# Optimization experiments

Measured on AMD Instinct MI355X. Metric: run time of the kernel, lower is better.

The kernel has to match this reference:

```python
import jax, jax.numpy as jnp
import numpy as np
import math

NUM_HEADS = 16
MAX_REL_POS = 128


def setup_inputs() -> dict:
    key = jax.random.key(0)
    ks = jax.random.split(key, 6)
    B, S, H = 4, 1024, 1024
    hd = H // NUM_HEADS
    sc = 1.0 / math.sqrt(H)
    return {
        "x": jax.random.normal(ks[0], (B, S, H), jnp.float32),
        "Wq": jax.random.normal(ks[1], (H, H), jnp.float32) * sc,
        "bq": jnp.zeros((H,), jnp.float32),
        "Wk": jax.random.normal(ks[2], (H, H), jnp.float32) * sc,
        "bk": jnp.zeros((H,), jnp.float32),
        "Wv": jax.random.normal(ks[3], (H, H), jnp.float32) * sc,
        "bv": jnp.zeros((H,), jnp.float32),
        "Wo": jax.random.normal(ks[4], (H, H), jnp.float32) * sc,
        "bo": jnp.zeros((H,), jnp.float32),
        "rel_emb": jax.random.normal(ks[5], (2 * MAX_REL_POS + 1, hd), jnp.float32) * 0.02,
    }


def reference(x, Wq, bq, Wk, bk, Wv, bv, Wo, bo, rel_emb):
    B, S, H = x.shape
    nh = NUM_HEADS
    hd = H // nh
    inv_sqrt_d = 1.0 / math.sqrt(hd)

    # torch Linear: y = x @ W.T + b; reshape to [B, nh, S, hd]
    def proj(W, b):
        return (x @ W.T + b).reshape(B, S, nh, hd).transpose(0, 2, 1, 3)

    Q = proj(Wq, bq)
    K = proj(Wk, bk)
    V = proj(Wv, bv)

    # relative position indices, clipped to [-max_rel_pos, max_rel_pos]
    pos = jnp.arange(S)
    rel_idx = jnp.clip(pos[None, :] - pos[:, None], -MAX_REL_POS, MAX_REL_POS) + MAX_REL_POS
    E = rel_emb[rel_idx]  # [S, S, hd]

    # content scores + learned relative-position bias, both scaled by 1/sqrt(hd)
    scores = (jnp.einsum('bnqd,bnkd->bnqk', Q, K)
              + jnp.einsum('bnqd,qkd->bnqk', Q, E)) * inv_sqrt_d
    attn = jax.nn.softmax(scores, axis=-1)

    out = jnp.einsum('bnqk,bnkd->bnqd', attn, V)  # [B, nh, S, hd]
    out = out.transpose(0, 2, 1, 3).reshape(B, S, H)
    return out @ Wo.T + bo
```

## Files before the change

### kernel.cpp

```cpp
#include <hip/hip_runtime.h>
#include <math.h>

#define S_LEN 1024
#define NREL  257
#define QRST  272

typedef _Float16 f16;
typedef __attribute__((ext_vector_type(8))) _Float16 f16x8;
typedef __attribute__((ext_vector_type(4))) float f32x4;

__device__ inline void load_lds_16(const void* g, void* l) {
    __builtin_amdgcn_global_load_lds(
        (const __attribute__((address_space(1))) void*)g,
        (__attribute__((address_space(3))) void*)l, 16, 0, 0);
}

__global__ __launch_bounds__(256)
void convert_f16(const float* __restrict__ src, f16* __restrict__ dst)
{
    const int t = blockIdx.x * 256 + threadIdx.x;
    const int row128 = t & 127;
    const int kc     = (t >> 7) & 3;
    const int ktile  = (t >> 9) & 31;
    const int mtile  = t >> 14;
    const float* s = src + ((size_t)(mtile * 128 + row128) * 1024) + ktile * 32 + kc * 8;
    float4 v0 = *reinterpret_cast<const float4*>(s);
    float4 v1 = *reinterpret_cast<const float4*>(s + 4);
    float v[8] = {v0.x, v0.y, v0.z, v0.w, v1.x, v1.y, v1.z, v1.w};
    union { f16 h[8]; int4 q; } H;
    #pragma unroll
    for (int i = 0; i < 8; ++i) H.h[i] = (f16)v[i];
    reinterpret_cast<int4*>(dst)[t] = H.q;
}

__global__ __launch_bounds__(256)
void convert_w(const float* __restrict__ Wq, const float* __restrict__ Wk,
               const float* __restrict__ Wv, const float* __restrict__ Wo,
               f16* __restrict__ wqkv, f16* __restrict__ wo)
{
    const int y = blockIdx.y;
    const float* src = (y == 0) ? Wq : (y == 1) ? Wk : (y == 2) ? Wv : Wo;
    f16* dst = (y < 3) ? (wqkv + (size_t)y * 1048576) : wo;
    const int t = blockIdx.x * 256 + threadIdx.x;
    const int row128 = t & 127;
    const int kc     = (t >> 7) & 3;
    const int ktile  = (t >> 9) & 31;
    const int mtile  = t >> 14;
    const float* s = src + ((size_t)(mtile * 128 + row128) * 1024) + ktile * 32 + kc * 8;
    float4 v0 = *reinterpret_cast<const float4*>(s);
    float4 v1 = *reinterpret_cast<const float4*>(s + 4);
    float v[8] = {v0.x, v0.y, v0.z, v0.w, v1.x, v1.y, v1.z, v1.w};
    union { f16 h[8]; int4 q; } H;
    #pragma unroll
    for (int i = 0; i < 8; ++i) H.h[i] = (f16)v[i];
    reinterpret_cast<int4*>(dst)[t] = H.q;
}

__global__ __launch_bounds__(256)
void rel_convert(const float* __restrict__ rel, f16* __restrict__ relc)
{
    const int t = blockIdx.x * 256 + threadIdx.x;
    const int ck = t / 272, row = t % 272;
    union { f16 h[8]; int4 q; } H;
    #pragma unroll
    for (int i = 0; i < 8; ++i) H.h[i] = (f16)0.f;
    if (ck < 8 && row < NREL) {
        const float* s = rel + (size_t)row * 64 + ck * 8;
        float4 v0 = *reinterpret_cast<const float4*>(s);
        float4 v1 = *reinterpret_cast<const float4*>(s + 4);
        float v[8] = {v0.x, v0.y, v0.z, v0.w, v1.x, v1.y, v1.z, v1.w};
        #pragma unroll
        for (int i = 0; i < 8; ++i) H.h[i] = (f16)v[i];
    }
    reinterpret_cast<int4*>(relc)[t] = H.q;
}

__global__ __launch_bounds__(256)
void gemm_qkv(const f16* __restrict__ Ah, const f16* __restrict__ Bh,
              const float* __restrict__ bq, const float* __restrict__ bk,
              const float* __restrict__ bv,
              f16* __restrict__ Qout, f16* __restrict__ Kt, f16* __restrict__ Vt)
{
    __shared__ __align__(16) f16 sm[2][2][4096];
    const int tid  = threadIdx.x;
    const int wave = tid >> 6, lane = tid & 63;
    const int wm = wave >> 1, wn = wave & 1;
    const int r16 = lane & 15, kq = lane >> 4;
    const int mtile = blockIdx.y;
    const int ntile = blockIdx.x;
    const int wb = (tid & ~63) << 3;

    f32x4 acc[4][4] = {};

    auto stage = [&](int buf, int kt) {
        const f16* gA = Ah + ((size_t)(mtile * 32 + kt) << 12);
        const f16* gB = Bh + ((size_t)(ntile * 32 + kt) << 12);
        load_lds_16(gA + ((size_t)tid << 3),         &sm[buf][0][wb]);
        load_lds_16(gA + ((size_t)(tid + 256) << 3), &sm[buf][0][wb + 2048]);
        load_lds_16(gB + ((size_t)tid << 3),         &sm[buf][1][wb]);
        load_lds_16(gB + ((size_t)(tid + 256) << 3), &sm[buf][1][wb + 2048]);
    };

    stage(0, 0);
    __syncthreads();

    for (int kt = 0; kt < 32; ++kt) {
        const int cur = kt & 1;
        if (kt + 1 < 32) stage(cur ^ 1, kt + 1);

        const f16x8* pA = reinterpret_cast<const f16x8*>(sm[cur][0]);
        const f16x8* pB = reinterpret_cast<const f16x8*>(sm[cur][1]);

        f16x8 af[4], bf[4];
        #pragma unroll
        for (int m = 0; m < 4; ++m) af[m] = pA[kq * 128 + wm * 64 + m * 16 + r16];
        #pragma unroll
        for (int n = 0; n < 4; ++n) bf[n] = pB[kq * 128 + wn * 64 + n * 16 + r16];
        #pragma unroll
        for (int m = 0; m < 4; ++m)
            #pragma unroll
            for (int n = 0; n < 4; ++n)
                acc[m][n] = __builtin_amdgcn_mfma_f32_16x16x32_f16(af[m], bf[n], acc[m][n], 0, 0, 0);
        __syncthreads();
    }

    const int nsel = ntile >> 3;
    const float scale = (nsel == 0) ? 0.125f : 1.0f;
    const float* bp = (nsel == 0) ? bq : ((nsel == 1) ? bk : bv);
    const int row0 = (mtile << 7) + wm * 64;
    const int col0 = ((ntile & 7) << 7) + wn * 64;

    #pragma unroll
    for (int n = 0; n < 4; ++n) {
        const int col = col0 + n * 16 + r16;
        const float bc = bp[col];
        #pragma unroll
        for (int m = 0; m < 4; ++m) {
            #pragma unroll
            for (int r = 0; r < 4; ++r) {
                const int row = row0 + m * 16 + kq * 4 + r;
                const float val = (acc[m][n][r] + bc) * scale;
                const int b = row >> 10, s = row & 1023;
                const int nh = col >> 6, d = col & 63;
                if (nsel == 0) {
                    Qout[((((size_t)(b * 16 + nh)) << 10 | (size_t)s) << 6) + d] = (f16)val;
                } else if (nsel == 1) {
                    const size_t cidx = (((size_t)(b * 16 + nh) << 13) + ((s >> 6) << 9)
                                        + ((d >> 3) << 6) + (s & 63)) * 8 + (d & 7);
                    Kt[cidx] = (f16)val;
                } else {
                    const int kk = s & 63;
                    const size_t cidx = (((size_t)(b * 16 + nh) << 13) + ((s >> 6) << 9)
                                        + ((kk >> 3) << 6) + d) * 8 + (kk & 7);
                    Vt[cidx] = (f16)val;
                }
            }
        }
    }
}

__global__ __launch_bounds__(256)
void gemm_out(const f16* __restrict__ Ah, const f16* __restrict__ Bh,
              const float* __restrict__ bias, float* __restrict__ out)
{
    __shared__ __align__(16) f16 sm[2][6144];
    const int tid  = threadIdx.x;
    const int wave = tid >> 6, lane = tid & 63;
    const int wm = wave >> 1, wn = wave & 1;
    const int r16 = lane & 15, kq = lane >> 4;
    const int mtile = blockIdx.y;
    const int ntile = blockIdx.x;
    const int wb = (tid & ~63) << 3;

    f32x4 acc[4][2] = {};

    auto stage = [&](int buf, int kt) {
        const f16* gA = Ah + ((size_t)(mtile * 32 + kt) << 12);
        const f16* gB = Bh + ((size_t)((ntile >> 1) * 32 + kt) << 12) + ((ntile & 1) << 9);
        load_lds_16(gA + ((size_t)tid << 3),         &sm[buf][wb]);
        load_lds_16(gA + ((size_t)(tid + 256) << 3), &sm[buf][wb + 2048]);
        load_lds_16(gB + (((size_t)(tid >> 6)) << 10) + ((size_t)(tid & 63) << 3),
                    &sm[buf][4096 + wb]);
    };

    stage(0, 0);
    __syncthreads();

    for (int kt = 0; kt < 32; ++kt) {
        const int cur = kt & 1;
        if (kt + 1 < 32) stage(cur ^ 1, kt + 1);

        const f16x8* pA = reinterpret_cast<const f16x8*>(&sm[cur][0]);
        const f16x8* pB = reinterpret_cast<const f16x8*>(&sm[cur][4096]);

        f16x8 af[4], bf[2];
        #pragma unroll
        for (int m = 0; m < 4; ++m) af[m] = pA[kq * 128 + wm * 64 + m * 16 + r16];
        #pragma unroll
        for (int n = 0; n < 2; ++n) bf[n] = pB[kq * 64 + wn * 32 + n * 16 + r16];
        #pragma unroll
        for (int m = 0; m < 4; ++m)
            #pragma unroll
            for (int n = 0; n < 2; ++n)
                acc[m][n] = __builtin_amdgcn_mfma_f32_16x16x32_f16(af[m], bf[n], acc[m][n], 0, 0, 0);
        __syncthreads();
    }

    const int row0 = (mtile << 7) + wm * 64;
    const int col0 = (ntile << 6) + wn * 32;
    #pragma unroll
    for (int n = 0; n < 2; ++n) {
        const int col = col0 + n * 16 + r16;
        const float bc = bias[col];
        #pragma unroll
        for (int m = 0; m < 4; ++m)
            #pragma unroll
            for (int r = 0; r < 4; ++r) {
                const int row = row0 + m * 16 + kq * 4 + r;
                out[(size_t)row * 1024 + col] = acc[m][n][r] + bc;
            }
    }
}

__global__ __launch_bounds__(256)
void qrel_gemm(const f16* __restrict__ Qf, const f16* __restrict__ relc,
               f16* __restrict__ QR)
{
    __shared__ __align__(16) char lds[36864];
    const int tid = threadIdx.x;
    const int w = tid >> 6, l = tid & 63;
    const int r16 = l & 15, kq = l >> 4;
    const int blk = blockIdx.x;
    const int wb = (tid & 192) << 4;

    #pragma unroll
    for (int i = 0; i < 9; ++i)
        load_lds_16((const char*)relc + i * 4096 + tid * 16, lds + i * 4096 + wb);

    const int qrow = (blk << 6) + w * 16 + r16;
    f16x8 ah[2];
    ah[0] = *reinterpret_cast<const f16x8*>(Qf + (size_t)qrow * 64 + kq * 8);
    ah[1] = *reinterpret_cast<const f16x8*>(Qf + (size_t)qrow * 64 + 32 + kq * 8);

    __syncthreads();

    f32x4 S[17] = {};
    const f16x8* cB = reinterpret_cast<const f16x8*>(lds);
    #pragma unroll
    for (int c = 0; c < 2; ++c) {
        #pragma unroll
        for (int n = 0; n < 17; ++n) {
            const f16x8 bf = cB[(c * 4 + kq) * 272 + n * 16 + r16];
            S[n] = __builtin_amdgcn_mfma_f32_16x16x32_f16(ah[c], bf, S[n], 0, 0, 0);
        }
    }

    const int qbase = (blk << 6) + w * 16 + kq * 4;
    #pragma unroll
    for (int n = 0; n < 17; ++n) {
        const int col = n * 16 + r16;
        #pragma unroll
        for (int r = 0; r < 4; ++r)
            QR[(size_t)(qbase + r) * QRST + col] = (f16)S[n][r];
    }
}

__global__ __launch_bounds__(256, 2)
void attn_kernel(const f16* __restrict__ Qf, const f16* __restrict__ Kt,
                 const f16* __restrict__ Vt, const f16* __restrict__ QR,
                 f16* __restrict__ AO)
{
    __shared__ __align__(16) char lds[16384 + 128 * 68 * 4];
    float* P = (float*)(lds + 16384);

    const int id  = blockIdx.x;
    const int xcd = id & 7;
    const int j   = id >> 3;
    const int qt  = j & 7;
    const int bh  = ((j >> 3) << 3) | xcd;
    const int q0  = qt << 7;

    const int tid = threadIdx.x;
    const int w = tid >> 6;
    const int l = tid & 63;
    const int r16 = l & 15, kq = l >> 4;

    f16x8 qf[2][2];
    #pragma unroll
    for (int m = 0; m < 2; ++m) {
        const size_t qoff = (((size_t)bh << 10) + q0 + w * 32 + m * 16 + r16) * 64;
        #pragma unroll
        for (int c = 0; c < 2; ++c)
            qf[m][c] = *reinterpret_cast<const f16x8*>(Qf + qoff + c * 32 + kq * 8);
    }

    float qr_lo[2][4], qr_hi[2][4];
    #pragma unroll
    for (int m = 0; m < 2; ++m)
        #pragma unroll
        for (int r = 0; r < 4; ++r) {
            const f16* p = QR + (size_t)((bh << 10) + q0 + w * 32 + m * 16 + kq * 4 + r) * QRST;
            qr_lo[m][r] = (float)p[0];
            qr_hi[m][r] = (float)p[256];
        }

    float m_run[2][4] = {{-1e30f, -1e30f, -1e30f, -1e30f}, {-1e30f, -1e30f, -1e30f, -1e30f}};
    float l_run[2][4] = {};
    f32x4 accO[2][4] = {};

    const int wb = (tid & 192) << 4;

    for (int kt = 0; kt < S_LEN; kt += 64) {
        __syncthreads();

        {
            const size_t tbase = ((size_t)(bh * 16) + (kt >> 6)) * 8192;
            const char* gK = (const char*)Kt + tbase;
            const char* gV = (const char*)Vt + tbase;
            #pragma unroll
            for (int i = 0; i < 2; ++i) {
                load_lds_16(gK + i * 4096 + tid * 16, lds + i * 4096 + wb);
                load_lds_16(gV + i * 4096 + tid * 16, lds + 8192 + i * 4096 + wb);
            }
        }

        float bias[2][4][4];
        if (kt - q0 >= 256) {
            #pragma unroll
            for (int m = 0; m < 2; ++m)
                #pragma unroll
                for (int n = 0; n < 4; ++n)
                    #pragma unroll
                    for (int r = 0; r < 4; ++r) bias[m][n][r] = qr_hi[m][r];
        } else if (q0 - kt >= 192) {
            #pragma unroll
            for (int m = 0; m < 2; ++m)
                #pragma unroll
                for (int n = 0; n < 4; ++n)
                    #pragma unroll
                    for (int r = 0; r < 4; ++r) bias[m][n][r] = qr_lo[m][r];
        } else {
            #pragma unroll
            for (int m = 0; m < 2; ++m) {
                const int qb = q0 + w * 32 + m * 16 + kq * 4;
                const int base_d = kt - qb + 128 + r16;
                #pragma unroll
                for (int r = 0; r < 4; ++r) {
                    const f16* qrp = QR + (size_t)((bh << 10) + qb + r) * QRST;
                    #pragma unroll
                    for (int n = 0; n < 4; ++n) {
                        int dlt = base_d + n * 16 - r;
                        dlt = dlt < 0 ? 0 : (dlt > 256 ? 256 : dlt);
                        bias[m][n][r] = (float)qrp[dlt];
                    }
                }
            }
        }

        __syncthreads();

        f32x4 S[2][4] = {};
        const f16x8* cK = reinterpret_cast<const f16x8*>(lds);
        #pragma unroll
        for (int c = 0; c < 2; ++c) {
            f16x8 kf[4];
            #pragma unroll
            for (int n = 0; n < 4; ++n)
                kf[n] = cK[(c * 4 + kq) * 64 + n * 16 + r16];
            #pragma unroll
            for (int m = 0; m < 2; ++m)
                #pragma unroll
                for (int n = 0; n < 4; ++n)
                    S[m][n] = __builtin_amdgcn_mfma_f32_16x16x32_f16(qf[m][c], kf[n], S[m][n], 0, 0, 0);
        }

        #pragma unroll
        for (int m = 0; m < 2; ++m) {
            float pv[4][4];
            float tmax[4] = {-1e30f, -1e30f, -1e30f, -1e30f};
            #pragma unroll
            for (int n = 0; n < 4; ++n)
                #pragma unroll
                for (int r = 0; r < 4; ++r) {
                    const float s = S[m][n][r] + bias[m][n][r];
                    pv[n][r] = s;
                    tmax[r] = fmaxf(tmax[r], s);
                }
            #pragma unroll
            for (int r = 0; r < 4; ++r) {
                tmax[r] = fmaxf(tmax[r], __shfl_xor(tmax[r], 1));
                tmax[r] = fmaxf(tmax[r], __shfl_xor(tmax[r], 2));
                tmax[r] = fmaxf(tmax[r], __shfl_xor(tmax[r], 4));
                tmax[r] = fmaxf(tmax[r], __shfl_xor(tmax[r], 8));
            }
            float corr[4], psum[4] = {0.f, 0.f, 0.f, 0.f};
            #pragma unroll
            for (int r = 0; r < 4; ++r) {
                const float m_new = fmaxf(m_run[m][r], tmax[r]);
                corr[r] = __expf(m_run[m][r] - m_new);
                m_run[m][r] = m_new;
            }
            #pragma unroll
            for (int n = 0; n < 4; ++n)
                #pragma unroll
                for (int r = 0; r < 4; ++r) {
                    pv[n][r] = __expf(pv[n][r] - m_run[m][r]);
                    psum[r] += pv[n][r];
                }
            #pragma unroll
            for (int r = 0; r < 4; ++r) {
                psum[r] += __shfl_xor(psum[r], 1);
                psum[r] += __shfl_xor(psum[r], 2);
                psum[r] += __shfl_xor(psum[r], 4);
                psum[r] += __shfl_xor(psum[r], 8);
                l_run[m][r] = l_run[m][r] * corr[r] + psum[r];
            }
            #pragma unroll
            for (int n = 0; n < 4; ++n)
                #pragma unroll
                for (int r = 0; r < 4; ++r) accO[m][n][r] *= corr[r];

            #pragma unroll
            for (int n = 0; n < 4; ++n)
                #pragma unroll
                for (int r = 0; r < 4; ++r)
                    P[(w * 32 + m * 16 + kq * 4 + r) * 68 + n * 16 + r16] = pv[n][r];
        }

        __syncthreads();

        const f16x8* cV = reinterpret_cast<const f16x8*>(lds + 8192);
        #pragma unroll
        for (int m = 0; m < 2; ++m) {
            const int prow = (w * 32 + m * 16 + r16) * 68;
            #pragma unroll
            for (int c = 0; c < 2; ++c) {
                float4 p0 = *reinterpret_cast<const float4*>(&P[prow + c * 32 + kq * 8]);
                float4 p1 = *reinterpret_cast<const float4*>(&P[prow + c * 32 + kq * 8 + 4]);
                f16x8 pa;
                pa[0] = (f16)p0.x; pa[1] = (f16)p0.y; pa[2] = (f16)p0.z; pa[3] = (f16)p0.w;
                pa[4] = (f16)p1.x; pa[5] = (f16)p1.y; pa[6] = (f16)p1.z; pa[7] = (f16)p1.w;
                #pragma unroll
                for (int n = 0; n < 4; ++n) {
                    const f16x8 vf = cV[(c * 4 + kq) * 64 + n * 16 + r16];
                    accO[m][n] = __builtin_amdgcn_mfma_f32_16x16x32_f16(pa, vf, accO[m][n], 0, 0, 0);
                }
            }
        }
    }

    #pragma unroll
    for (int m = 0; m < 2; ++m) {
        float inv[4];
        #pragma unroll
        for (int r = 0; r < 4; ++r) inv[r] = 1.f / l_run[m][r];
        const int qs_base = q0 + w * 32 + m * 16 + kq * 4;
        #pragma unroll
        for (int n = 0; n < 4; ++n)
            #pragma unroll
            for (int r = 0; r < 4; ++r) {
                const float v = accO[m][n][r] * inv[r];
                const int r_g  = ((bh >> 4) << 10) + qs_base + r;
                const int kcol = ((bh & 15) << 6) + n * 16 + r16;
                const size_t idx = ((((size_t)(r_g >> 7) * 32 + (kcol >> 5)) * 4
                                    + ((kcol >> 3) & 3)) * 128 + (r_g & 127)) * 8 + (kcol & 7);
                AO[idx] = (f16)v;
            }
    }
}

extern "C" void kernel_launch(void* const* d_in, const int* in_sizes, int n_in,
                              void* d_out, int out_size, void* d_ws, size_t ws_size,
                              hipStream_t stream)
{
    const float* x   = (const float*)d_in[0];
    const float* Wq  = (const float*)d_in[1];
    const float* bq  = (const float*)d_in[2];
    const float* Wk  = (const float*)d_in[3];
    const float* bk  = (const float*)d_in[4];
    const float* Wv  = (const float*)d_in[5];
    const float* bv  = (const float*)d_in[6];
    const float* Wo  = (const float*)d_in[7];
    const float* bo  = (const float*)d_in[8];
    const float* rel = (const float*)d_in[9];
    float* out = (float*)d_out;

    char* W = (char*)d_ws;
    f16* Qf   = (f16*)(W);
    f16* QR   = (f16*)(W + 8388608);
    f16* Kt   = (f16*)(W + 44040192);
    f16* Vt   = (f16*)(W + 52428800);
    f16* xt   = (f16*)(W + 60817408);
    f16* wqkv = (f16*)(W + 69206016);
    f16* wo   = (f16*)(W + 75497472);
    f16* AO   = (f16*)(W + 77594624);
    f16* relc = (f16*)(W + 85983232);

    convert_f16<<<2048, 256, 0, stream>>>(x, xt);
    convert_w<<<dim3(512, 4), 256, 0, stream>>>(Wq, Wk, Wv, Wo, wqkv, wo);
    rel_convert<<<9, 256, 0, stream>>>(rel, relc);

    gemm_qkv<<<dim3(24, 32), dim3(256), 0, stream>>>(
        xt, wqkv, bq, bk, bv, Qf, Kt, Vt);

    qrel_gemm<<<1024, 256, 0, stream>>>(Qf, relc, QR);

    attn_kernel<<<512, 256, 0, stream>>>(Qf, Kt, Vt, QR, AO);

    gemm_out<<<dim3(16, 32), dim3(256), 0, stream>>>(AO, wo, bo, out);
}
```

Baseline: 258.5 us.

## Double-buffer K/V tiles, prefetch bias, store P as f16, MFMA row sums

Restructures the attention loop so the next K/V tile is loaded into a second LDS buffer and its relative-position bias is gathered while the current tile is computed. This removes one block barrier per iteration and hides global load latency. The softmax probabilities are now written to LDS as f16 instead of f32, halving P traffic and dropping the per-read conversion. The row-sum shuffle reduction is replaced by an extra MFMA against a ones vector. The trade-off is roughly 51 KB of LDS per block instead of about 51 KB split differently, more live registers for the prefetched bias, and a row sum taken from f16-rounded probabilities.

After: 219.3 us. -15.2%, faster.

```diff
diff --git a/kernel.cpp b/kernel.cpp
--- a/kernel.cpp
+++ b/kernel.cpp
@@ -270,8 +270,8 @@
                  const f16* __restrict__ Vt, const f16* __restrict__ QR,
                  f16* __restrict__ AO)
 {
-    __shared__ __align__(16) char lds[16384 + 128 * 68 * 4];
-    float* P = (float*)(lds + 16384);
+    __shared__ __align__(16) char lds[32768 + 128 * 72 * 2];
+    f16* Pf = (f16*)(lds + 32768);
 
     const int id  = blockIdx.x;
     const int xcd = id & 7;
@@ -284,6 +284,7 @@
     const int w = tid >> 6;
     const int l = tid & 63;
     const int r16 = l & 15, kq = l >> 4;
+    const int wb = (tid & 192) << 4;
 
     f16x8 qf[2][2];
     #pragma unroll
@@ -305,45 +306,41 @@
         }
 
     float m_run[2][4] = {{-1e30f, -1e30f, -1e30f, -1e30f}, {-1e30f, -1e30f, -1e30f, -1e30f}};
-    float l_run[2][4] = {};
     f32x4 accO[2][4] = {};
-
-    const int wb = (tid & 192) << 4;
-
-    for (int kt = 0; kt < S_LEN; kt += 64) {
-        __syncthreads();
-
-        {
-            const size_t tbase = ((size_t)(bh * 16) + (kt >> 6)) * 8192;
-            const char* gK = (const char*)Kt + tbase;
-            const char* gV = (const char*)Vt + tbase;
-            #pragma unroll
-            for (int i = 0; i < 2; ++i) {
-                load_lds_16(gK + i * 4096 + tid * 16, lds + i * 4096 + wb);
-                load_lds_16(gV + i * 4096 + tid * 16, lds + 8192 + i * 4096 + wb);
-            }
-        }
-
-        float bias[2][4][4];
-        if (kt - q0 >= 256) {
+    f32x4 acc_l[2] = {};
+
+    auto stage = [&](int buf, int t) {
+        const size_t tbase = ((size_t)(bh * 16) + t) * 8192;
+        const char* gK = (const char*)Kt + tbase;
+        const char* gV = (const char*)Vt + tbase;
+        #pragma unroll
+        for (int i = 0; i < 2; ++i) {
+            load_lds_16(gK + i * 4096 + tid * 16, lds + buf * 16384 + i * 4096 + wb);
+            load_lds_16(gV + i * 4096 + tid * 16, lds + buf * 16384 + 8192 + i * 4096 + wb);
+        }
+    };
+
+    auto gather = [&](int t, float (&bb)[2][4][4]) {
+        const int ktv = t << 6;
+        if (ktv - q0 >= 256) {
             #pragma unroll
             for (int m = 0; m < 2; ++m)
                 #pragma unroll
                 for (int n = 0; n < 4; ++n)
                     #pragma unroll
-                    for (int r = 0; r < 4; ++r) bias[m][n][r] = qr_hi[m][r];
-        } else if (q0 - kt >= 192) {
+                    for (int r = 0; r < 4; ++r) bb[m][n][r] = qr_hi[m][r];
+        } else if (q0 - ktv >= 192) {
             #pragma unroll
             for (int m = 0; m < 2; ++m)
                 #pragma unroll
                 for (int n = 0; n < 4; ++n)
                     #pragma unroll
-                    for (int r = 0; r < 4; ++r) bias[m][n][r] = qr_lo[m][r];
+                    for (int r = 0; r < 4; ++r) bb[m][n][r] = qr_lo[m][r];
         } else {
             #pragma unroll
             for (int m = 0; m < 2; ++m) {
                 const int qb = q0 + w * 32 + m * 16 + kq * 4;
-                const int base_d = kt - qb + 128 + r16;
+                const int base_d = ktv - qb + 128 + r16;
                 #pragma unroll
                 for (int r = 0; r < 4; ++r) {
                     const f16* qrp = QR + (size_t)((bh << 10) + qb + r) * QRST;
@@ -351,16 +348,31 @@
                     for (int n = 0; n < 4; ++n) {
                         int dlt = base_d + n * 16 - r;
                         dlt = dlt < 0 ? 0 : (dlt > 256 ? 256 : dlt);
-                        bias[m][n][r] = (float)qrp[dlt];
+                        bb[m][n][r] = (float)qrp[dlt];
                     }
                 }
             }
         }
-
-        __syncthreads();
+    };
+
+    float biasc[2][4][4];
+    stage(0, 0);
+    gather(0, biasc);
+    __syncthreads();
+
+    const f16x8 ones = {(f16)1.f, (f16)1.f, (f16)1.f, (f16)1.f,
+                        (f16)1.f, (f16)1.f, (f16)1.f, (f16)1.f};
+
+    for (int t = 0; t < 16; ++t) {
+        const int cur = t & 1;
+        float nb[2][4][4];
+        if (t + 1 < 16) {
+            stage(cur ^ 1, t + 1);
+            gather(t + 1, nb);
+        }
 
         f32x4 S[2][4] = {};
-        const f16x8* cK = reinterpret_cast<const f16x8*>(lds);
+        const f16x8* cK = reinterpret_cast<const f16x8*>(lds + cur * 16384);
         #pragma unroll
         for (int c = 0; c < 2; ++c) {
             f16x8 kf[4];
@@ -382,7 +394,7 @@
             for (int n = 0; n < 4; ++n)
                 #pragma unroll
                 for (int r = 0; r < 4; ++r) {
-                    const float s = S[m][n][r] + bias[m][n][r];
+                    const float s = S[m][n][r] + biasc[m][n][r];
                     pv[n][r] = s;
                     tmax[r] = fmaxf(tmax[r], s);
                 }
@@ -393,7 +405,7 @@
                 tmax[r] = fmaxf(tmax[r], __shfl_xor(tmax[r], 4));
                 tmax[r] = fmaxf(tmax[r], __shfl_xor(tmax[r], 8));
             }
-            float corr[4], psum[4] = {0.f, 0.f, 0.f, 0.f};
+            float corr[4];
             #pragma unroll
             for (int r = 0; r < 4; ++r) {
                 const float m_new = fmaxf(m_run[m][r], tmax[r]);
@@ -403,49 +415,47 @@
             #pragma unroll
             for (int n = 0; n < 4; ++n)
                 #pragma unroll
-                for (int r = 0; r < 4; ++r) {
+                for (int r = 0; r < 4; ++r)
                     pv[n][r] = __expf(pv[n][r] - m_run[m][r]);
-                    psum[r] += pv[n][r];
-                }
-            #pragma unroll
-            for (int r = 0; r < 4; ++r) {
-                psum[r] += __shfl_xor(psum[r], 1);
-                psum[r] += __shfl_xor(psum[r], 2);
-                psum[r] += __shfl_xor(psum[r], 4);
-                psum[r] += __shfl_xor(psum[r], 8);
-                l_run[m][r] = l_run[m][r] * corr[r] + psum[r];
-            }
             #pragma unroll
             for (int n = 0; n < 4; ++n)
                 #pragma unroll
                 for (int r = 0; r < 4; ++r) accO[m][n][r] *= corr[r];
+            #pragma unroll
+            for (int r = 0; r < 4; ++r) acc_l[m][r] *= corr[r];
 
             #pragma unroll
             for (int n = 0; n < 4; ++n)
                 #pragma unroll
                 for (int r = 0; r < 4; ++r)
-                    P[(w * 32 + m * 16 + kq * 4 + r) * 68 + n * 16 + r16] = pv[n][r];
-        }
-
-        __syncthreads();
-
-        const f16x8* cV = reinterpret_cast<const f16x8*>(lds + 8192);
+                    Pf[(w * 32 + m * 16 + kq * 4 + r) * 72 + n * 16 + r16] = (f16)pv[n][r];
+        }
+
+        const f16x8* cV = reinterpret_cast<const f16x8*>(lds + cur * 16384 + 8192);
         #pragma unroll
         for (int m = 0; m < 2; ++m) {
-            const int prow = (w * 32 + m * 16 + r16) * 68;
+            const int prow = (w * 32 + m * 16 + r16) * 72;
             #pragma unroll
             for (int c = 0; c < 2; ++c) {
-                float4 p0 = *reinterpret_cast<const float4*>(&P[prow + c * 32 + kq * 8]);
-                float4 p1 = *reinterpret_cast<const float4*>(&P[prow + c * 32 + kq * 8 + 4]);
-                f16x8 pa;
-                pa[0] = (f16)p0.x; pa[1] = (f16)p0.y; pa[2] = (f16)p0.z; pa[3] = (f16)p0.w;
-                pa[4] = (f16)p1.x; pa[5] = (f16)p1.y; pa[6] = (f16)p1.z; pa[7] = (f16)p1.w;
+                const f16x8 pa = *reinterpret_cast<const f16x8*>(&Pf[prow + c * 32 + kq * 8]);
                 #pragma unroll
                 for (int n = 0; n < 4; ++n) {
                     const f16x8 vf = cV[(c * 4 + kq) * 64 + n * 16 + r16];
                     accO[m][n] = __builtin_amdgcn_mfma_f32_16x16x32_f16(pa, vf, accO[m][n], 0, 0, 0);
                 }
-            }
+                acc_l[m] = __builtin_amdgcn_mfma_f32_16x16x32_f16(pa, ones, acc_l[m], 0, 0, 0);
+            }
+        }
+
+        __syncthreads();
+
+        if (t + 1 < 16) {
+            #pragma unroll
+            for (int m = 0; m < 2; ++m)
+                #pragma unroll
+                for (int n = 0; n < 4; ++n)
+                    #pragma unroll
+                    for (int r = 0; r < 4; ++r) biasc[m][n][r] = nb[m][n][r];
         }
     }
 
@@ -453,7 +463,7 @@
     for (int m = 0; m < 2; ++m) {
         float inv[4];
         #pragma unroll
-        for (int r = 0; r < 4; ++r) inv[r] = 1.f / l_run[m][r];
+        for (int r = 0; r < 4; ++r) inv[r] = 1.f / acc_l[m][r];
         const int qs_base = q0 + w * 32 + m * 16 + kq * 4;
         #pragma unroll
         for (int n = 0; n < 4; ++n)
```
